# Kernel optimization log

Hardware: AMD Instinct MI355X
Metric: run time of the kernel (lower is better)

The kernel has to match this reference:

```python
import jax, jax.numpy as jnp
import numpy as np

B, N, E, H = 16, 768, 1024, 16  # batch == heads so mask[i] (head-indexed, as in the source) is valid
D = E // H
MASK_P = 0.1
NEG = jnp.float32(-1e16)


def setup_inputs() -> dict:
    key = jax.random.key(0)
    ks = jax.random.split(key, 8)
    query = jax.random.normal(ks[0], (B, N, E), jnp.float32)
    key_t = jax.random.normal(ks[1], (B, N, E), jnp.float32)
    value = jax.random.normal(ks[2], (B, N, E), jnp.float32)
    u = jax.random.uniform(ks[3], (B, N))
    mask = jnp.where(u < MASK_P, -jnp.inf, 0.0).astype(jnp.float32)
    # per-head Linear(head_dim, head_dim, bias=False) weights, stacked over heads: (H, out=D, in=D)
    Wq = jax.random.normal(ks[4], (H, D, D), jnp.float32) * (1.0 / np.sqrt(D))
    Wk = jax.random.normal(ks[5], (H, D, D), jnp.float32) * (1.0 / np.sqrt(D))
    Wv = jax.random.normal(ks[6], (H, D, D), jnp.float32) * (1.0 / np.sqrt(D))
    Wf = jax.random.normal(ks[7], (E, E), jnp.float32) * (1.0 / np.sqrt(E))
    return {"query": query, "key": key_t, "value": value, "mask": mask,
            "Wq": Wq, "Wk": Wk, "Wv": Wv, "Wf": Wf}


def reference(query, key, value, mask, Wq, Wk, Wv, Wf):
    b, n, e = query.shape
    h = Wq.shape[0]
    d = e // h
    q = query.reshape(b, n, h, d)
    k = key.reshape(b, n, h, d)
    v = value.reshape(b, n, h, d)
    # per-head nn.Linear: x @ W[i].T  (W: (H, out, in))
    qh = jnp.einsum('bnhd,hed->bnhe', q, Wq)
    kh = jnp.einsum('bnhd,hed->bnhe', k, Wk)
    vh = jnp.einsum('bnhd,hed->bnhe', v, Wv)
    # scaled QK^T: divide by embed_size**0.5 (NOT head_dim) as in the source
    scores = jnp.einsum('bqhd,bkhd->bhqk', qh, kh) / jnp.sqrt(jnp.float32(e))  # (B,H,N,N)
    # faithful quirk: mask row selected by HEAD index i -> same additive mask for all batches
    bad = jnp.isneginf(mask)[:h]                      # (H, N)
    add = jnp.where(bad[:, :, None] | bad[:, None, :], NEG, jnp.float32(0.0))  # (H,N,N): row/col blanked
    probs = jax.nn.softmax(scores + add[None], axis=-1)
    attn = jnp.einsum('bhqk,bkhd->bqhd', probs, vh)   # (B,N,H,D)
    out = attn.reshape(b, n, e) @ Wf.T
    return out
```

## Files before the change

### kernel.cpp

```cpp
#include <hip/hip_runtime.h>

#define B_ 16
#define N_ 768
#define E_ 1024
#define H_ 16
#define D_ 64

typedef __bf16 bf16x8 __attribute__((ext_vector_type(8)));
typedef float f32x4 __attribute__((ext_vector_type(4)));
typedef unsigned short ushort8 __attribute__((ext_vector_type(8)));
typedef unsigned short ushort4v __attribute__((ext_vector_type(4)));
typedef unsigned int uint2v __attribute__((ext_vector_type(2)));
typedef unsigned int uint4v __attribute__((ext_vector_type(4)));

__device__ __forceinline__ unsigned short f2bf(float x) {
  unsigned u = __builtin_bit_cast(unsigned, x);
  u += 0x7FFFu + ((u >> 16) & 1u);
  return (unsigned short)(u >> 16);
}

__device__ __forceinline__ unsigned cvtpk(float lo, float hi) {
  unsigned r;
  asm("v_cvt_pk_bf16_f32 %0, %1, %2" : "=v"(r) : "v"(lo), "v"(hi));
  return r;
}

__device__ __forceinline__ float fexp2(float x) {
  float r;
  asm("v_exp_f32 %0, %1" : "=v"(r) : "v"(x));
  return r;
}

__device__ __forceinline__ f32x4 mfma16(ushort8 a, ushort8 b, f32x4 c) {
  return __builtin_amdgcn_mfma_f32_16x16x32_bf16(
      __builtin_bit_cast(bf16x8, a), __builtin_bit_cast(bf16x8, b), c, 0, 0, 0);
}

__global__ __launch_bounds__(256, 1) void proj_kernel(
    const float* __restrict__ q, const float* __restrict__ k, const float* __restrict__ v,
    const float* __restrict__ Wq, const float* __restrict__ Wk, const float* __restrict__ Wv,
    const float* __restrict__ Wf, unsigned short* __restrict__ Qh,
    unsigned short* __restrict__ Kh, unsigned short* __restrict__ Vt,
    unsigned short* __restrict__ Wfb) {
  const int m = blockIdx.x / 3072;
  const int rest = blockIdx.x - m * 3072;
  const int nt = rest % 12;
  const int bh = rest / 12;
  const int b = bh >> 4, h = bh & 15;
  const int tid = threadIdx.x;
  const int w = tid >> 6, l = tid & 63;
  const int l16 = l & 15, lg = l >> 4;

  __shared__ __align__(16) unsigned short Xs[64][72];
  __shared__ __align__(16) unsigned short Ws[64][72];

  const float* xp = (m == 0) ? q : (m == 1) ? k : v;
  const float* wp = ((m == 0) ? Wq : (m == 1) ? Wk : Wv) + (size_t)h * 4096;

  const int row = tid >> 4;
  const int c4 = (tid & 15) * 4;

  float4 xt[4], wt[4];
#pragma unroll
  for (int i = 0; i < 4; ++i)
    xt[i] = *(const float4*)&xp[((size_t)(b * N_ + nt * 64 + i * 16 + row)) * E_ + h * 64 + c4];
#pragma unroll
  for (int i = 0; i < 4; ++i)
    wt[i] = *(const float4*)&wp[(i * 16 + row) * 64 + c4];

  float4 wfv;
  if (blockIdx.x < 1024)
    wfv = *(const float4*)&Wf[((size_t)blockIdx.x * 256 + tid) * 4];

#pragma unroll
  for (int i = 0; i < 4; ++i) {
    ushort4v s;
    s[0] = f2bf(xt[i].x); s[1] = f2bf(xt[i].y); s[2] = f2bf(xt[i].z); s[3] = f2bf(xt[i].w);
    *(ushort4v*)&Xs[i * 16 + row][c4] = s;
  }
#pragma unroll
  for (int i = 0; i < 4; ++i) {
    ushort4v s;
    s[0] = f2bf(wt[i].x); s[1] = f2bf(wt[i].y); s[2] = f2bf(wt[i].z); s[3] = f2bf(wt[i].w);
    *(ushort4v*)&Ws[i * 16 + row][c4] = s;
  }
  if (blockIdx.x < 1024) {
    ushort4v s;
    s[0] = f2bf(wfv.x); s[1] = f2bf(wfv.y); s[2] = f2bf(wfv.z); s[3] = f2bf(wfv.w);
    *(ushort4v*)&Wfb[((size_t)blockIdx.x * 256 + tid) * 4] = s;
  }
  __syncthreads();

  f32x4 acc[4] = {};
#pragma unroll
  for (int kc = 0; kc < 2; ++kc) {
    ushort8 a = *(const ushort8*)&Xs[w * 16 + l16][kc * 32 + lg * 8];
#pragma unroll
    for (int eg = 0; eg < 4; ++eg) {
      ushort8 bf = *(const ushort8*)&Ws[eg * 16 + l16][kc * 32 + lg * 8];
      acc[eg] = mfma16(a, bf, acc[eg]);
    }
  }

  if (m < 2) {
    unsigned short* op = (m == 0) ? Qh : Kh;
    __syncthreads();
#pragma unroll
    for (int eg = 0; eg < 4; ++eg)
#pragma unroll
      for (int r = 0; r < 4; ++r)
        Xs[w * 16 + lg * 4 + r][eg * 16 + l16] = f2bf(acc[eg][r]);
    __syncthreads();
#pragma unroll
    for (int i = 0; i < 2; ++i) {
      int rw = i * 32 + (tid >> 3), c8 = (tid & 7) * 8;
      *(ushort8*)&op[((size_t)(b * H_ + h) * N_ + nt * 64 + rw) * 64 + c8] =
          *(const ushort8*)&Xs[rw][c8];
    }
  } else {
    __syncthreads();
#pragma unroll
    for (int eg = 0; eg < 4; ++eg) {
      uint2v pk;
      pk[0] = cvtpk(acc[eg][0], acc[eg][1]);
      pk[1] = cvtpk(acc[eg][2], acc[eg][3]);
      *(uint2v*)&Xs[eg * 16 + l16][w * 16 + lg * 4] = pk;
    }
    __syncthreads();
#pragma unroll
    for (int i = 0; i < 2; ++i) {
      int rw = i * 32 + (tid >> 3), c8 = (tid & 7) * 8;
      *(ushort8*)&Vt[((size_t)bh * 64 + rw) * N_ + nt * 64 + c8] =
          *(const ushort8*)&Xs[rw][c8];
    }
  }
}

__global__ __launch_bounds__(256, 4) void attn_kernel(
    const unsigned short* __restrict__ Qh, const unsigned short* __restrict__ Kh,
    const unsigned short* __restrict__ Vt, const float* __restrict__ mask,
    unsigned short* __restrict__ attnO) {
  const int bid = blockIdx.x;
  const int logical = (bid & 7) * 192 + (bid >> 3);
  const int qt = logical % 6;
  const int bh = logical / 6;
  const int b = bh >> 4, h = bh & 15;
  const int tid = threadIdx.x;
  const int w = tid >> 6, l = tid & 63;
  const int l16 = l & 15, lg = l >> 4;

  __shared__ __align__(16) unsigned short Ks[64][72];
  __shared__ __align__(16) unsigned short Vs[64][72];
  __shared__ __align__(16) unsigned short Ps[4][32][72];
  __shared__ float addk[N_];

  const size_t baseK = (size_t)bh * N_ * 64;
  const size_t baseV = (size_t)bh * 64 * N_;
  const int qrow0 = qt * 128 + w * 32;
  const float C2 = 0.04508422f;

  for (int i = tid; i < N_; i += 256)
    addk[i] = (mask[h * N_ + i] < -1e30f) ? -1.0e20f : 0.0f;

  ushort8 bQ[2][2];
#pragma unroll
  for (int qs = 0; qs < 2; ++qs)
#pragma unroll
    for (int kc = 0; kc < 2; ++kc)
      bQ[qs][kc] = *(const ushort8*)&Qh[((size_t)bh * N_ + qrow0 + qs * 16 + l16) * 64 +
                                        kc * 32 + lg * 8];
  float bqf[2];
#pragma unroll
  for (int qs = 0; qs < 2; ++qs)
    bqf[qs] = (mask[h * N_ + qrow0 + qs * 16 + l16] < -1e30f) ? 1.f : 0.f;

  const int srow = tid >> 3;
  const int sc8 = (tid & 7) * 8;

  uint4v kreg[2], vreg[2];
#pragma unroll
  for (int i = 0; i < 2; ++i) {
    int row = i * 32 + srow;
    kreg[i] = *(const uint4v*)&Kh[baseK + (size_t)row * 64 + sc8];
    vreg[i] = *(const uint4v*)&Vt[baseV + (size_t)row * N_ + sc8];
  }
  __syncthreads();
#pragma unroll
  for (int i = 0; i < 2; ++i) {
    int row = i * 32 + srow;
    *(ushort8*)&Ks[row][sc8] = __builtin_bit_cast(ushort8, kreg[i]);
    *(ushort8*)&Vs[row][sc8] = __builtin_bit_cast(ushort8, vreg[i]);
  }
  __syncthreads();

  f32x4 oacc[2][4] = {};
  float l_part[2] = {0.f, 0.f};

  for (int kt = 0; kt < 12; ++kt) {
    if (kt < 11) {
#pragma unroll
      for (int i = 0; i < 2; ++i) {
        int row = i * 32 + srow;
        kreg[i] = *(const uint4v*)&Kh[baseK + (size_t)((kt + 1) * 64 + row) * 64 + sc8];
        vreg[i] = *(const uint4v*)&Vt[baseV + (size_t)row * N_ + (kt + 1) * 64 + sc8];
      }
    }

#pragma unroll
    for (int cg = 0; cg < 4; ++cg) {
      f32x4 st[2] = {};
#pragma unroll
      for (int kc = 0; kc < 2; ++kc) {
        ushort8 aK = *(const ushort8*)&Ks[cg * 16 + l16][kc * 32 + lg * 8];
        st[0] = mfma16(aK, bQ[0][kc], st[0]);
        st[1] = mfma16(aK, bQ[1][kc], st[1]);
      }
      f32x4 ak4 = *(const f32x4*)&addk[kt * 64 + cg * 16 + lg * 4];
#pragma unroll
      for (int qs = 0; qs < 2; ++qs) {
        float p[4];
#pragma unroll
        for (int r = 0; r < 4; ++r) {
          float t = __builtin_fmaf(st[qs][r], C2, ak4[r]);
          t = (bqf[qs] > 0.f) ? 0.0f : t;
          p[r] = fexp2(t);
          l_part[qs] += p[r];
        }
        uint2v pk;
        pk[0] = cvtpk(p[0], p[1]);
        pk[1] = cvtpk(p[2], p[3]);
        *(uint2v*)&Ps[w][qs * 16 + l16][cg * 16 + lg * 4] = pk;
      }
    }

#pragma unroll
    for (int kc = 0; kc < 2; ++kc) {
      ushort8 ap[2];
#pragma unroll
      for (int qs = 0; qs < 2; ++qs)
        ap[qs] = *(const ushort8*)&Ps[w][qs * 16 + l16][kc * 32 + lg * 8];
#pragma unroll
      for (int dg = 0; dg < 4; ++dg) {
        ushort8 bv = *(const ushort8*)&Vs[dg * 16 + l16][kc * 32 + lg * 8];
        oacc[0][dg] = mfma16(ap[0], bv, oacc[0][dg]);
        oacc[1][dg] = mfma16(ap[1], bv, oacc[1][dg]);
      }
    }

    __syncthreads();
    if (kt < 11) {
#pragma unroll
      for (int i = 0; i < 2; ++i) {
        int row = i * 32 + srow;
        *(ushort8*)&Ks[row][sc8] = __builtin_bit_cast(ushort8, kreg[i]);
        *(ushort8*)&Vs[row][sc8] = __builtin_bit_cast(ushort8, vreg[i]);
      }
    }
    __syncthreads();
  }

#pragma unroll
  for (int qs = 0; qs < 2; ++qs) {
    float s = l_part[qs];
    s += __shfl_xor(s, 16);
    s += __shfl_xor(s, 32);
#pragma unroll
    for (int r = 0; r < 4; ++r) {
      float dnm = __shfl(s, lg * 4 + r);
      float inv = 1.f / dnm;
      int qg = qrow0 + qs * 16 + lg * 4 + r;
      size_t orow = ((size_t)b * N_ + qg) * E_ + h * 64;
#pragma unroll
      for (int dg = 0; dg < 4; ++dg)
        attnO[orow + dg * 16 + l16] = f2bf(oacc[qs][dg][r] * inv);
    }
  }
}

__global__ __launch_bounds__(256) void gemm_kernel(const unsigned short* __restrict__ A,
                                                   const unsigned short* __restrict__ Bm,
                                                   float* __restrict__ out) {
  const int be = blockIdx.x & 7;
  const int bm = blockIdx.x >> 3;
  const int tid = threadIdx.x;
  const int w = tid >> 6, l = tid & 63;
  const int l16 = l & 15, lg = l >> 4;
  const int wm = w >> 1, wn = w & 1;

  __shared__ __align__(16) unsigned short As[128][72];
  __shared__ __align__(16) unsigned short Bs[128][72];

  f32x4 acc[4][4] = {};
  const int m0 = bm * 128, e0 = be * 128;
  const int srow = tid >> 3, sc8 = (tid & 7) * 8;
  const unsigned short* Ab = A + (size_t)(m0 + srow) * E_ + sc8;
  const unsigned short* Bb = Bm + (size_t)(e0 + srow) * E_ + sc8;

  uint4v ar[4], br[4];
#pragma unroll
  for (int i = 0; i < 4; ++i) {
    ar[i] = *(const uint4v*)(Ab + (size_t)i * 32 * E_);
    br[i] = *(const uint4v*)(Bb + (size_t)i * 32 * E_);
  }

  for (int kk = 0; kk < 16; ++kk) {
    __syncthreads();
#pragma unroll
    for (int i = 0; i < 4; ++i) {
      *(ushort8*)&As[i * 32 + srow][sc8] = __builtin_bit_cast(ushort8, ar[i]);
      *(ushort8*)&Bs[i * 32 + srow][sc8] = __builtin_bit_cast(ushort8, br[i]);
    }
    __syncthreads();
    if (kk < 15) {
#pragma unroll
      for (int i = 0; i < 4; ++i) {
        ar[i] = *(const uint4v*)(Ab + (size_t)i * 32 * E_ + (kk + 1) * 64);
        br[i] = *(const uint4v*)(Bb + (size_t)i * 32 * E_ + (kk + 1) * 64);
      }
    }
#pragma unroll
    for (int kc = 0; kc < 2; ++kc) {
      ushort8 a[4], bf[4];
#pragma unroll
      for (int i = 0; i < 4; ++i)
        a[i] = *(const ushort8*)&As[wm * 64 + i * 16 + l16][kc * 32 + lg * 8];
#pragma unroll
      for (int j = 0; j < 4; ++j)
        bf[j] = *(const ushort8*)&Bs[wn * 64 + j * 16 + l16][kc * 32 + lg * 8];
#pragma unroll
      for (int i = 0; i < 4; ++i)
#pragma unroll
        for (int j = 0; j < 4; ++j) acc[i][j] = mfma16(a[i], bf[j], acc[i][j]);
    }
  }

#pragma unroll
  for (int i = 0; i < 4; ++i)
#pragma unroll
    for (int j = 0; j < 4; ++j)
#pragma unroll
      for (int r = 0; r < 4; ++r)
        out[(size_t)(m0 + wm * 64 + i * 16 + lg * 4 + r) * E_ + e0 + wn * 64 + j * 16 + l16] =
            acc[i][j][r];
}

extern "C" void kernel_launch(void* const* d_in, const int* in_sizes, int n_in,
                              void* d_out, int out_size, void* d_ws, size_t ws_size,
                              hipStream_t stream) {
  const float* q = (const float*)d_in[0];
  const float* k = (const float*)d_in[1];
  const float* v = (const float*)d_in[2];
  const float* mask = (const float*)d_in[3];
  const float* Wq = (const float*)d_in[4];
  const float* Wk = (const float*)d_in[5];
  const float* Wv = (const float*)d_in[6];
  const float* Wf = (const float*)d_in[7];
  float* out = (float*)d_out;

  const size_t PH = (size_t)B_ * H_ * N_ * D_;
  unsigned short* Qh = (unsigned short*)d_ws;
  unsigned short* Kh = Qh + PH;
  unsigned short* Vt = Kh + PH;
  unsigned short* attn = Vt + PH;
  unsigned short* Wfb = attn + PH;

  proj_kernel<<<3 * B_ * H_ * (N_ / 64), 256, 0, stream>>>(q, k, v, Wq, Wk, Wv, Wf, Qh, Kh,
                                                           Vt, Wfb);
  attn_kernel<<<B_ * H_ * (N_ / 128), 256, 0, stream>>>(Qh, Kh, Vt, mask, attn);
  gemm_kernel<<<(B_ * N_ / 128) * (E_ / 128), 256, 0, stream>>>(attn, Wfb, out);
}
```

Baseline: 140.8 us.

## Keep softmax probabilities in registers using permlane swaps instead of LDS round-trip

Computes all four score column groups up front, then repacks the exponentiated probabilities into the MFMA A-operand layout in registers with v_permlane32/16_swap. This replaces the per-warp LDS store and reload of P, removing LDS traffic and the shared Ps buffer. The cost is higher register pressure from holding 8 score accumulators at once, plus dependence on the swap-based lane mapping being correct.

```diff
diff --git a/kernel.cpp b/kernel.cpp
--- a/kernel.cpp
+++ b/kernel.cpp
@@ -151,7 +151,6 @@
 
   __shared__ __align__(16) unsigned short Ks[64][72];
   __shared__ __align__(16) unsigned short Vs[64][72];
-  __shared__ __align__(16) unsigned short Ps[4][32][72];
   __shared__ float addk[N_];
 
   const size_t baseK = (size_t)bh * N_ * 64;
@@ -206,44 +205,55 @@
       }
     }
 
+    f32x4 st[4][2] = {};
+#pragma unroll
+    for (int kc = 0; kc < 2; ++kc) {
+#pragma unroll
+      for (int cg = 0; cg < 4; ++cg) {
+        ushort8 aK = *(const ushort8*)&Ks[cg * 16 + l16][kc * 32 + lg * 8];
+        st[cg][0] = mfma16(aK, bQ[0][kc], st[cg][0]);
+        st[cg][1] = mfma16(aK, bQ[1][kc], st[cg][1]);
+      }
+    }
+
 #pragma unroll
     for (int cg = 0; cg < 4; ++cg) {
-      f32x4 st[2] = {};
-#pragma unroll
-      for (int kc = 0; kc < 2; ++kc) {
-        ushort8 aK = *(const ushort8*)&Ks[cg * 16 + l16][kc * 32 + lg * 8];
-        st[0] = mfma16(aK, bQ[0][kc], st[0]);
-        st[1] = mfma16(aK, bQ[1][kc], st[1]);
-      }
       f32x4 ak4 = *(const f32x4*)&addk[kt * 64 + cg * 16 + lg * 4];
 #pragma unroll
       for (int qs = 0; qs < 2; ++qs) {
-        float p[4];
 #pragma unroll
         for (int r = 0; r < 4; ++r) {
-          float t = __builtin_fmaf(st[qs][r], C2, ak4[r]);
+          float t = __builtin_fmaf(st[cg][qs][r], C2, ak4[r]);
           t = (bqf[qs] > 0.f) ? 0.0f : t;
-          p[r] = fexp2(t);
-          l_part[qs] += p[r];
+          float p = fexp2(t);
+          l_part[qs] += p;
+          st[cg][qs][r] = p;
         }
-        uint2v pk;
-        pk[0] = cvtpk(p[0], p[1]);
-        pk[1] = cvtpk(p[2], p[3]);
-        *(uint2v*)&Ps[w][qs * 16 + l16][cg * 16 + lg * 4] = pk;
-      }
-    }
-
-#pragma unroll
-    for (int kc = 0; kc < 2; ++kc) {
-      ushort8 ap[2];
-#pragma unroll
-      for (int qs = 0; qs < 2; ++qs)
-        ap[qs] = *(const ushort8*)&Ps[w][qs * 16 + l16][kc * 32 + lg * 8];
+      }
+    }
+
+#pragma unroll
+    for (int kcP = 0; kcP < 2; ++kcP) {
+      ushort8 pa[2];
+#pragma unroll
+      for (int qs = 0; qs < 2; ++qs) {
+        unsigned a0 = cvtpk(st[2 * kcP][qs][0], st[2 * kcP][qs][1]);
+        unsigned b0 = cvtpk(st[2 * kcP][qs][2], st[2 * kcP][qs][3]);
+        unsigned a1 = cvtpk(st[2 * kcP + 1][qs][0], st[2 * kcP + 1][qs][1]);
+        unsigned b1 = cvtpk(st[2 * kcP + 1][qs][2], st[2 * kcP + 1][qs][3]);
+        asm("v_permlane32_swap_b32 %0, %1" : "+v"(a0), "+v"(a1));
+        asm("v_permlane16_swap_b32 %0, %1" : "+v"(a0), "+v"(a1));
+        asm("v_permlane32_swap_b32 %0, %1" : "+v"(b0), "+v"(b1));
+        asm("v_permlane16_swap_b32 %0, %1" : "+v"(b0), "+v"(b1));
+        uint4v pk;
+        pk[0] = a0; pk[1] = b0; pk[2] = a1; pk[3] = b1;
+        pa[qs] = __builtin_bit_cast(ushort8, pk);
+      }
 #pragma unroll
       for (int dg = 0; dg < 4; ++dg) {
-        ushort8 bv = *(const ushort8*)&Vs[dg * 16 + l16][kc * 32 + lg * 8];
-        oacc[0][dg] = mfma16(ap[0], bv, oacc[0][dg]);
-        oacc[1][dg] = mfma16(ap[1], bv, oacc[1][dg]);
+        ushort8 bv = *(const ushort8*)&Vs[dg * 16 + l16][kcP * 32 + lg * 8];
+        oacc[0][dg] = mfma16(pa[0], bv, oacc[0][dg]);
+        oacc[1][dg] = mfma16(pa[1], bv, oacc[1][dg]);
       }
     }
 
```

After: 136.6 us. -3.0%, faster.
